# Kernel tuning notes

Measured on AMD Instinct MI355X. Metric: run time of the kernel, lower is better.

## Reference

```python
import jax, jax.numpy as jnp
import numpy as np

N, CDIM, FDIM, HDIM, K = 16384, 512, 512, 1024, 5
WEIGHT = 5.0
EPS = 1e-20


def _xavier(key, shape, gain):
    fan_in, fan_out = shape[-2], shape[-1]
    std = gain * np.sqrt(2.0 / (fan_in + fan_out))
    return jax.random.normal(key, shape, jnp.float32) * std


def setup_inputs() -> dict:
    key = jax.random.key(0)
    ks = jax.random.split(key, 12)
    g = np.sqrt(2.0)  # relu gain; last layer linear gain=1
    inp = {
        "c": jax.random.normal(ks[0], (N, CDIM), jnp.float32),
        "x": jax.random.normal(ks[1], (N, 3), jnp.float32),
        "noise": jax.random.normal(ks[2], (K, N, FDIM), jnp.float32),
        "gumbel_u": jax.random.uniform(ks[3], (N, K), jnp.float32),
        # probs MLP: cdim -> 1024 -> 1024 -> K
        "pw0": _xavier(ks[4], (CDIM, HDIM), g), "pb0": jnp.zeros((HDIM,), jnp.float32),
        "pw1": _xavier(ks[5], (HDIM, HDIM), g), "pb1": jnp.zeros((HDIM,), jnp.float32),
        "pw2": _xavier(ks[6], (HDIM, K), 1.0), "pb2": jnp.zeros((K,), jnp.float32),
        # K Gaussian MLPs (stacked): cdim -> 1024 -> 1024 -> 2*fdim
        "gw0": _xavier(ks[7], (K, CDIM, HDIM), g), "gb0": jnp.zeros((K, HDIM), jnp.float32),
        "gw1": _xavier(ks[8], (K, HDIM, HDIM), g), "gb1": jnp.zeros((K, HDIM), jnp.float32),
        "gw2": _xavier(ks[9], (K, HDIM, 2 * FDIM), 1.0), "gb2": jnp.zeros((K, 2 * FDIM), jnp.float32),
    }
    return inp


def reference(c, x, noise, gumbel_u, pw0, pb0, pw1, pb1, pw2, pb2,
              gw0, gb0, gw1, gb1, gw2, gb2):
    # mixture probabilities: ps = softmax(probs(c))
    h = jax.nn.relu(c @ pw0 + pb0)
    h = jax.nn.relu(h @ pw1 + pb1)
    logits = h @ pw2 + pb2                      # (N, K)
    ps = jax.nn.softmax(logits, axis=-1)

    # all K Gaussian experts, vectorized over component axis k
    g = jax.nn.relu(jnp.einsum('nc,kch->knh', c, gw0) + gb0[:, None, :])
    g = jax.nn.relu(jnp.einsum('knh,khj->knj', g, gw1) + gb1[:, None, :])
    o = jnp.einsum('knh,khf->knf', g, gw2) + gb2[:, None, :]   # (K, N, 2*FDIM)
    mean, logvar = o[..., :FDIM], o[..., FDIM:]
    sample = mean + noise * jnp.exp(logvar * 0.5)              # (K, N, FDIM)

    # per-row categorical draw with p = ps (Gumbel-max, on-device)
    gumbel = -jnp.log(-jnp.log(gumbel_u + EPS) + EPS)
    idx = jnp.argmax(jnp.log(jax.lax.stop_gradient(ps) + EPS) + gumbel, axis=-1)

    mask = jax.nn.one_hot(idx, K, dtype=ps.dtype) * WEIGHT
    weights = (ps + mask) / (1.0 + WEIGHT)                     # (N, K)
    out = jnp.einsum('nk,knf->nf', weights, sample)            # (N, FDIM)
    return out
```

## Files before the change

### kernel.cpp

```cpp
#include <hip/hip_runtime.h>
#include <cstdint>
#include <cstddef>

#define N_ROWS 16384
#define CDIM_C 512
#define HDIM_C 1024
#define FDIM_C 512
#define KMIX 5

typedef unsigned short u16;
typedef __attribute__((ext_vector_type(8))) short bf16x8;
typedef __attribute__((ext_vector_type(4))) float f32x4;

__device__ __forceinline__ u16 f2bf(float x) {
  unsigned u = __float_as_uint(x);
  unsigned r = (u + 0x7fffu + ((u >> 16) & 1u)) >> 16;
  return (u16)r;
}
__device__ __forceinline__ float bf2f(u16 h) {
  return __uint_as_float(((unsigned)h) << 16);
}

__device__ __forceinline__ void gload_lds16(const void* g, void* l) {
  __builtin_amdgcn_global_load_lds((const __attribute__((address_space(1))) void*)g,
                                   (__attribute__((address_space(3))) void*)l,
                                   16, 0, 0);
}

__global__ void split3_kernel(const float* __restrict__ x, u16* __restrict__ P0,
                              u16* __restrict__ P1, u16* __restrict__ P2, size_t n) {
  for (size_t i = (size_t)blockIdx.x * 256 + threadIdx.x; i < n; i += (size_t)gridDim.x * 256) {
    const float v = x[i];
    const u16 h = f2bf(v); const float hf = bf2f(h);
    const u16 m = f2bf(v - hf); const float mf = bf2f(m);
    P0[i] = h; P1[i] = m; P2[i] = f2bf(v - hf - mf);
  }
}

template <int NP>
__global__ void transp_split_kernel(const float* __restrict__ W, u16* __restrict__ P0,
                                    u16* __restrict__ P1, u16* __restrict__ P2,
                                    int R, int C) {
  __shared__ float t[32][33];
  const int bz = blockIdx.z;
  const float* Wz = W + (size_t)bz * R * C;
  const size_t oofs = (size_t)bz * R * C;
  const int r0 = blockIdx.x * 32, c0 = blockIdx.y * 32;
  const int tx = threadIdx.x, ty = threadIdx.y;
#pragma unroll
  for (int i = 0; i < 4; ++i)
    t[ty + i * 8][tx] = Wz[(size_t)(r0 + ty + i * 8) * C + c0 + tx];
  __syncthreads();
#pragma unroll
  for (int i = 0; i < 4; ++i) {
    const int c = c0 + ty + i * 8, r = r0 + tx;
    const float x = t[tx][ty + i * 8];
    const size_t idx = oofs + (size_t)c * R + r;
    const u16 h = f2bf(x);
    P0[idx] = h;
    const float hf = bf2f(h);
    const u16 m = f2bf(x - hf);
    P1[idx] = m;
    if (NP >= 3) {
      const float mf = bf2f(m);
      P2[idx] = f2bf(x - hf - mf);
    }
  }
}

template <int NA, int NB, int NT, bool RELU, int OSPL>
__global__ __launch_bounds__(256, 2) void gemm_split(
    const u16* __restrict__ A0, const u16* __restrict__ A1, const u16* __restrict__ A2,
    const u16* __restrict__ B0, const u16* __restrict__ B1, const u16* __restrict__ B2,
    const float* __restrict__ bias, float* __restrict__ outF,
    u16* __restrict__ O0, u16* __restrict__ O1, u16* __restrict__ O2,
    int M, int Nc, int Kd) {
  __shared__ u16 lds[(NA + NB) * 4096];
  const int tid = threadIdx.x;
  const int lane = tid & 63;
  const int wave = tid >> 6;
  const int wm = wave >> 1, wn = wave & 1;
  const int col0 = blockIdx.x * 128;
  const int row0 = blockIdx.y * 128;
  const u16* Ap[3] = {A0, A1, A2};
  const u16* Bp[3] = {B0, B1, B2};
  constexpr int TA[6] = {0, 0, 1, 1, 0, 2};
  constexpr int TB[6] = {0, 1, 0, 1, 2, 0};

  f32x4 acc[4][4] = {};
  const int kb = lane >> 4;
  const int rl = lane & 15;
  const int nSteps = Kd >> 5;

  for (int kt = 0; kt < nSteps; ++kt) {
    const int k0 = kt << 5;
    __syncthreads();
#pragma unroll
    for (int p = 0; p < NA + NB; ++p) {
      const u16* gp = (p < NA) ? Ap[p] : Bp[p - NA];
      const int rb = (p < NA) ? row0 : col0;
      u16* lbase = &lds[p * 4096];
#pragma unroll
      for (int it = 0; it < 2; ++it) {
        const int sbase = it * 256 + wave * 64;
        const int slot = sbase + lane;
        const int skb = slot >> 7;
        const int sr = slot & 127;
        const u16* src = gp + (size_t)(rb + sr) * Kd + (k0 + skb * 8);
        gload_lds16(src, lbase + sbase * 8);
      }
    }
    __syncthreads();

    bf16x8 aF[NA][4];
    bf16x8 bF[NB][4];
#pragma unroll
    for (int p = 0; p < NA; ++p)
#pragma unroll
      for (int i = 0; i < 4; ++i) {
        const int r = wm * 64 + i * 16 + rl;
        aF[p][i] = *(const bf16x8*)&lds[p * 4096 + (kb * 128 + r) * 8];
      }
#pragma unroll
    for (int p = 0; p < NB; ++p)
#pragma unroll
      for (int j = 0; j < 4; ++j) {
        const int r = wn * 64 + j * 16 + rl;
        bF[p][j] = *(const bf16x8*)&lds[(NA + p) * 4096 + (kb * 128 + r) * 8];
      }
#pragma unroll
    for (int t = 0; t < NT; ++t)
#pragma unroll
      for (int i = 0; i < 4; ++i)
#pragma unroll
        for (int j = 0; j < 4; ++j)
          acc[i][j] = __builtin_amdgcn_mfma_f32_16x16x32_bf16(
              aF[TA[t]][i], bF[TB[t]][j], acc[i][j], 0, 0, 0);
  }

#pragma unroll
  for (int i = 0; i < 4; ++i)
#pragma unroll
    for (int j = 0; j < 4; ++j)
#pragma unroll
      for (int r = 0; r < 4; ++r) {
        const int row = row0 + wm * 64 + i * 16 + (lane >> 4) * 4 + r;
        const int col = col0 + wn * 64 + j * 16 + (lane & 15);
        float y = acc[i][j][r] + bias[col];
        if (RELU) y = fmaxf(y, 0.0f);
        const size_t idx = (size_t)row * Nc + col;
        if constexpr (OSPL == 0) {
          outF[idx] = y;
        } else {
          const u16 h = f2bf(y);
          const float hf = bf2f(h);
          const u16 m = f2bf(y - hf);
          O0[idx] = h;
          O1[idx] = m;
          if constexpr (OSPL == 3) {
            const float mf = bf2f(m);
            O2[idx] = f2bf(y - hf - mf);
          }
        }
      }
  (void)M;
}

__global__ void p2_weights_kernel(const float* __restrict__ h2, const float* __restrict__ pw2,
                                  const float* __restrict__ pb2, const float* __restrict__ gu,
                                  float* __restrict__ w) {
  const int n = blockIdx.x * 4 + (threadIdx.x >> 6);
  const int lane = threadIdx.x & 63;
  const float* hrow = h2 + (size_t)n * HDIM_C;
  double acc[KMIX] = {0, 0, 0, 0, 0};
  const int c0 = lane * 16;
#pragma unroll
  for (int jj = 0; jj < 16; ++jj) {
    const int cc = c0 + jj;
    const double hv = (double)hrow[cc];
#pragma unroll
    for (int kk = 0; kk < KMIX; ++kk)
      acc[kk] += hv * (double)pw2[cc * KMIX + kk];
  }
#pragma unroll
  for (int offs = 32; offs >= 1; offs >>= 1)
#pragma unroll
    for (int kk = 0; kk < KMIX; ++kk)
      acc[kk] += __shfl_down(acc[kk], offs);
  if (lane == 0) {
    double lg[KMIX], mx = -1e300;
#pragma unroll
    for (int kk = 0; kk < KMIX; ++kk) {
      lg[kk] = acc[kk] + (double)pb2[kk];
      if (lg[kk] > mx) mx = lg[kk];
    }
    double e[KMIX], s = 0.0;
#pragma unroll
    for (int kk = 0; kk < KMIX; ++kk) { e[kk] = exp(lg[kk] - mx); s += e[kk]; }
    int idx = 0; double zb = -1e300;
#pragma unroll
    for (int kk = 0; kk < KMIX; ++kk) {
      const double ps = e[kk] / s;
      const double u = (double)gu[n * KMIX + kk];
      const double g = -log(-log(u + 1e-20) + 1e-20);
      const double zz = log(ps + 1e-20) + g;
      if (zz > zb) { zb = zz; idx = kk; }
    }
#pragma unroll
    for (int kk = 0; kk < KMIX; ++kk)
      w[n * KMIX + kk] = (float)((e[kk] / s + (kk == idx ? 5.0 : 0.0)) / 6.0);
  }
}

template <bool FIRST>
__global__ void mix_kernel(const float* __restrict__ o, const float* __restrict__ nz,
                           const float* __restrict__ w, float* __restrict__ out, int k) {
  const int i = blockIdx.x * 256 + threadIdx.x;
  const int n = i >> 7;
  const int fv = i & 127;
  const float wk = w[n * KMIX + k];
  const float4 me = *(const float4*)(o + (size_t)n * HDIM_C + fv * 4);
  const float4 lv = *(const float4*)(o + (size_t)n * HDIM_C + FDIM_C + fv * 4);
  const float4 nv = *(const float4*)(nz + (size_t)n * FDIM_C + fv * 4);
  float4 r;
  r.x = wk * (me.x + nv.x * expf(0.5f * lv.x));
  r.y = wk * (me.y + nv.y * expf(0.5f * lv.y));
  r.z = wk * (me.z + nv.z * expf(0.5f * lv.z));
  r.w = wk * (me.w + nv.w * expf(0.5f * lv.w));
  float4* op = (float4*)out + i;
  if (FIRST) {
    *op = r;
  } else {
    float4 p = *op;
    p.x += r.x; p.y += r.y; p.z += r.z; p.w += r.w;
    *op = p;
  }
}

extern "C" void kernel_launch(void* const* d_in, const int* in_sizes, int n_in,
                              void* d_out, int out_size, void* d_ws, size_t ws_size,
                              hipStream_t stream) {
  const float* c   = (const float*)d_in[0];
  const float* noise = (const float*)d_in[2];
  const float* gu  = (const float*)d_in[3];
  const float* pw0 = (const float*)d_in[4];
  const float* pb0 = (const float*)d_in[5];
  const float* pw1 = (const float*)d_in[6];
  const float* pb1 = (const float*)d_in[7];
  const float* pw2 = (const float*)d_in[8];
  const float* pb2 = (const float*)d_in[9];
  const float* gw0 = (const float*)d_in[10];
  const float* gb0 = (const float*)d_in[11];
  const float* gw1 = (const float*)d_in[12];
  const float* gb1 = (const float*)d_in[13];
  const float* gw2 = (const float*)d_in[14];
  const float* gb2 = (const float*)d_in[15];
  float* out = (float*)d_out;

  char* ws = (char*)d_ws;
  size_t off = 0;
  auto alloc = [&](size_t bytes) -> char* {
    off = (off + 255) & ~(size_t)255;
    char* p = ws + off;
    off += bytes;
    return p;
  };

  const size_t NCp = (size_t)N_ROWS * CDIM_C * 2;
  const size_t NHp = (size_t)N_ROWS * HDIM_C * 2;
  u16* cH = (u16*)alloc(NCp);
  u16* cM = (u16*)alloc(NCp);
  u16* cL = (u16*)alloc(NCp);
  u16* pw0T0 = (u16*)alloc((size_t)CDIM_C * HDIM_C * 2);
  u16* pw0T1 = (u16*)alloc((size_t)CDIM_C * HDIM_C * 2);
  u16* pw0T2 = (u16*)alloc((size_t)CDIM_C * HDIM_C * 2);
  u16* pw1T0 = (u16*)alloc((size_t)HDIM_C * HDIM_C * 2);
  u16* pw1T1 = (u16*)alloc((size_t)HDIM_C * HDIM_C * 2);
  u16* pw1T2 = (u16*)alloc((size_t)HDIM_C * HDIM_C * 2);
  u16* hH = (u16*)alloc(NHp);
  u16* hM = (u16*)alloc(NHp);
  u16* hL = (u16*)alloc(NHp);
  float* h2 = (float*)alloc((size_t)N_ROWS * HDIM_C * 4);
  float* wbuf = (float*)alloc((size_t)N_ROWS * KMIX * 4);
  u16* gw0T0 = (u16*)alloc((size_t)KMIX * CDIM_C * HDIM_C * 2);
  u16* gw0T1 = (u16*)alloc((size_t)KMIX * CDIM_C * HDIM_C * 2);
  u16* gw1T0 = (u16*)alloc((size_t)KMIX * HDIM_C * HDIM_C * 2);
  u16* gw1T1 = (u16*)alloc((size_t)KMIX * HDIM_C * HDIM_C * 2);
  u16* gw2T0 = (u16*)alloc((size_t)KMIX * HDIM_C * HDIM_C * 2);
  u16* gw2T1 = (u16*)alloc((size_t)KMIX * HDIM_C * HDIM_C * 2);
  u16* g2b = (u16*)alloc(NHp);
  u16* g1a = hH;
  u16* g1b = hM;
  u16* g2a = hL;
  float* obuf = h2;
  (void)ws_size; (void)in_sizes; (void)n_in; (void)out_size;

  split3_kernel<<<2048, 256, 0, stream>>>(c, cH, cM, cL, (size_t)N_ROWS * CDIM_C);
  transp_split_kernel<3><<<dim3(CDIM_C / 32, HDIM_C / 32, 1), dim3(32, 8), 0, stream>>>(
      pw0, pw0T0, pw0T1, pw0T2, CDIM_C, HDIM_C);
  transp_split_kernel<3><<<dim3(HDIM_C / 32, HDIM_C / 32, 1), dim3(32, 8), 0, stream>>>(
      pw1, pw1T0, pw1T1, pw1T2, HDIM_C, HDIM_C);
  transp_split_kernel<2><<<dim3(CDIM_C / 32, HDIM_C / 32, KMIX), dim3(32, 8), 0, stream>>>(
      gw0, gw0T0, gw0T1, nullptr, CDIM_C, HDIM_C);
  transp_split_kernel<2><<<dim3(HDIM_C / 32, HDIM_C / 32, KMIX), dim3(32, 8), 0, stream>>>(
      gw1, gw1T0, gw1T1, nullptr, HDIM_C, HDIM_C);
  transp_split_kernel<2><<<dim3(HDIM_C / 32, HDIM_C / 32, KMIX), dim3(32, 8), 0, stream>>>(
      gw2, gw2T0, gw2T1, nullptr, HDIM_C, HDIM_C);

  const dim3 gg(HDIM_C / 128, N_ROWS / 128);

  gemm_split<3, 3, 6, true, 3><<<gg, 256, 0, stream>>>(
      cH, cM, cL, pw0T0, pw0T1, pw0T2, pb0, nullptr, hH, hM, hL,
      N_ROWS, HDIM_C, CDIM_C);
  gemm_split<3, 3, 6, true, 0><<<gg, 256, 0, stream>>>(
      hH, hM, hL, pw1T0, pw1T1, pw1T2, pb1, h2, nullptr, nullptr, nullptr,
      N_ROWS, HDIM_C, HDIM_C);
  p2_weights_kernel<<<N_ROWS / 4, 256, 0, stream>>>(h2, pw2, pb2, gu, wbuf);

  for (int k = 0; k < KMIX; ++k) {
    gemm_split<2, 2, 3, true, 2><<<gg, 256, 0, stream>>>(
        cH, cM, nullptr,
        gw0T0 + (size_t)k * CDIM_C * HDIM_C, gw0T1 + (size_t)k * CDIM_C * HDIM_C, nullptr,
        gb0 + k * HDIM_C, nullptr, g1a, g1b, nullptr,
        N_ROWS, HDIM_C, CDIM_C);
    gemm_split<2, 2, 3, true, 2><<<gg, 256, 0, stream>>>(
        g1a, g1b, nullptr,
        gw1T0 + (size_t)k * HDIM_C * HDIM_C, gw1T1 + (size_t)k * HDIM_C * HDIM_C, nullptr,
        gb1 + k * HDIM_C, nullptr, g2a, g2b, nullptr,
        N_ROWS, HDIM_C, HDIM_C);
    gemm_split<2, 2, 3, false, 0><<<gg, 256, 0, stream>>>(
        g2a, g2b, nullptr,
        gw2T0 + (size_t)k * HDIM_C * HDIM_C, gw2T1 + (size_t)k * HDIM_C * HDIM_C, nullptr,
        gb2 + k * HDIM_C, obuf, nullptr, nullptr, nullptr,
        N_ROWS, HDIM_C, HDIM_C);
    if (k == 0)
      mix_kernel<true><<<N_ROWS * 128 / 256, 256, 0, stream>>>(
          obuf, noise + (size_t)k * N_ROWS * FDIM_C, wbuf, out, k);
    else
      mix_kernel<false><<<N_ROWS * 128 / 256, 256, 0, stream>>>(
          obuf, noise + (size_t)k * N_ROWS * FDIM_C, wbuf, out, k);
  }
}
```

Measured before the change: 2.639 ms.

## Fuse mixture sampling into last expert GEMM epilogue and swizzle workgroups

The columns of the last-layer expert weights are interleaved during transposition, so each mean/logvar pair lands in adjacent lanes. The GEMM epilogue then computes the reparameterised sample with a lane shuffle and accumulates the weighted result into the output directly. This removes the separate mix kernel and the full fp32 round trip of the expert output. It also adds an XCD-style workgroup remap for L2 locality and raises launch-bounds occupancy hints (3 or 4 blocks per CU), which risks register spills. Half the epilogue lanes sit idle and the output stores become strided.

```diff
diff --git a/kernel.cpp b/kernel.cpp
--- a/kernel.cpp
+++ b/kernel.cpp
@@ -37,7 +37,7 @@
   }
 }
 
-template <int NP>
+template <int NP, bool PERM>
 __global__ void transp_split_kernel(const float* __restrict__ W, u16* __restrict__ P0,
                                     u16* __restrict__ P1, u16* __restrict__ P2,
                                     int R, int C) {
@@ -53,7 +53,8 @@
   __syncthreads();
 #pragma unroll
   for (int i = 0; i < 4; ++i) {
-    const int c = c0 + ty + i * 8, r = r0 + tx;
+    const int c_raw = c0 + ty + i * 8, r = r0 + tx;
+    const int c = PERM ? ((c_raw < FDIM_C) ? (c_raw * 2) : ((c_raw - FDIM_C) * 2 + 1)) : c_raw;
     const float x = t[tx][ty + i * 8];
     const size_t idx = oofs + (size_t)c * R + r;
     const u16 h = f2bf(x);
@@ -68,20 +69,28 @@
   }
 }
 
-template <int NA, int NB, int NT, bool RELU, int OSPL>
-__global__ __launch_bounds__(256, 2) void gemm_split(
+template <int NA, int NB, int NT, bool RELU, int OSPL, int MIX, int BPC>
+__global__ __launch_bounds__(256, BPC) void gemm_split(
     const u16* __restrict__ A0, const u16* __restrict__ A1, const u16* __restrict__ A2,
     const u16* __restrict__ B0, const u16* __restrict__ B1, const u16* __restrict__ B2,
     const float* __restrict__ bias, float* __restrict__ outF,
     u16* __restrict__ O0, u16* __restrict__ O1, u16* __restrict__ O2,
+    const float* __restrict__ noise_k, const float* __restrict__ wvec,
+    float* __restrict__ mixout, int kidx,
     int M, int Nc, int Kd) {
   __shared__ u16 lds[(NA + NB) * 4096];
   const int tid = threadIdx.x;
   const int lane = tid & 63;
   const int wave = tid >> 6;
   const int wm = wave >> 1, wn = wave & 1;
-  const int col0 = blockIdx.x * 128;
-  const int row0 = blockIdx.y * 128;
+
+  const int nwg = (int)(gridDim.x * gridDim.y);
+  const int orig = (int)(blockIdx.y * gridDim.x + blockIdx.x);
+  const int cpx = nwg >> 3;
+  const int wg = (orig & 7) * cpx + (orig >> 3);
+  const int col0 = (wg & 7) * 128;
+  const int row0 = (wg >> 3) * 128;
+
   const u16* Ap[3] = {A0, A1, A2};
   const u16* Bp[3] = {B0, B1, B2};
   constexpr int TA[6] = {0, 0, 1, 1, 0, 2};
@@ -146,20 +155,33 @@
       for (int r = 0; r < 4; ++r) {
         const int row = row0 + wm * 64 + i * 16 + (lane >> 4) * 4 + r;
         const int col = col0 + wn * 64 + j * 16 + (lane & 15);
-        float y = acc[i][j][r] + bias[col];
-        if (RELU) y = fmaxf(y, 0.0f);
-        const size_t idx = (size_t)row * Nc + col;
-        if constexpr (OSPL == 0) {
-          outF[idx] = y;
+        if constexpr (MIX > 0) {
+          const int f = col >> 1;
+          const int ocol = (col & 1) ? (f + FDIM_C) : f;
+          const float y = acc[i][j][r] + bias[ocol];
+          const float other = __shfl_xor(y, 1);
+          if (!(lane & 1)) {
+            const float sample = y + noise_k[(size_t)row * FDIM_C + f] * expf(0.5f * other);
+            const float v = wvec[row * KMIX + kidx] * sample;
+            float* op = &mixout[(size_t)row * FDIM_C + f];
+            if constexpr (MIX == 1) *op = v; else *op += v;
+          }
         } else {
-          const u16 h = f2bf(y);
-          const float hf = bf2f(h);
-          const u16 m = f2bf(y - hf);
-          O0[idx] = h;
-          O1[idx] = m;
-          if constexpr (OSPL == 3) {
-            const float mf = bf2f(m);
-            O2[idx] = f2bf(y - hf - mf);
+          float y = acc[i][j][r] + bias[col];
+          if (RELU) y = fmaxf(y, 0.0f);
+          const size_t idx = (size_t)row * Nc + col;
+          if constexpr (OSPL == 0) {
+            outF[idx] = y;
+          } else {
+            const u16 h = f2bf(y);
+            const float hf = bf2f(h);
+            const u16 m = f2bf(y - hf);
+            O0[idx] = h;
+            O1[idx] = m;
+            if constexpr (OSPL == 3) {
+              const float mf = bf2f(m);
+              O2[idx] = f2bf(y - hf - mf);
+            }
           }
         }
       }
@@ -209,31 +231,6 @@
 #pragma unroll
     for (int kk = 0; kk < KMIX; ++kk)
       w[n * KMIX + kk] = (float)((e[kk] / s + (kk == idx ? 5.0 : 0.0)) / 6.0);
-  }
-}
-
-template <bool FIRST>
-__global__ void mix_kernel(const float* __restrict__ o, const float* __restrict__ nz,
-                           const float* __restrict__ w, float* __restrict__ out, int k) {
-  const int i = blockIdx.x * 256 + threadIdx.x;
-  const int n = i >> 7;
-  const int fv = i & 127;
-  const float wk = w[n * KMIX + k];
-  const float4 me = *(const float4*)(o + (size_t)n * HDIM_C + fv * 4);
-  const float4 lv = *(const float4*)(o + (size_t)n * HDIM_C + FDIM_C + fv * 4);
-  const float4 nv = *(const float4*)(nz + (size_t)n * FDIM_C + fv * 4);
-  float4 r;
-  r.x = wk * (me.x + nv.x * expf(0.5f * lv.x));
-  r.y = wk * (me.y + nv.y * expf(0.5f * lv.y));
-  r.z = wk * (me.z + nv.z * expf(0.5f * lv.z));
-  r.w = wk * (me.w + nv.w * expf(0.5f * lv.w));
-  float4* op = (float4*)out + i;
-  if (FIRST) {
-    *op = r;
-  } else {
-    float4 p = *op;
-    p.x += r.x; p.y += r.y; p.z += r.z; p.w += r.w;
-    *op = p;
   }
 }
 
@@ -292,52 +289,52 @@
   u16* g1a = hH;
   u16* g1b = hM;
   u16* g2a = hL;
-  float* obuf = h2;
   (void)ws_size; (void)in_sizes; (void)n_in; (void)out_size;
 
   split3_kernel<<<2048, 256, 0, stream>>>(c, cH, cM, cL, (size_t)N_ROWS * CDIM_C);
-  transp_split_kernel<3><<<dim3(CDIM_C / 32, HDIM_C / 32, 1), dim3(32, 8), 0, stream>>>(
+  transp_split_kernel<3, false><<<dim3(CDIM_C / 32, HDIM_C / 32, 1), dim3(32, 8), 0, stream>>>(
       pw0, pw0T0, pw0T1, pw0T2, CDIM_C, HDIM_C);
-  transp_split_kernel<3><<<dim3(HDIM_C / 32, HDIM_C / 32, 1), dim3(32, 8), 0, stream>>>(
+  transp_split_kernel<3, false><<<dim3(HDIM_C / 32, HDIM_C / 32, 1), dim3(32, 8), 0, stream>>>(
       pw1, pw1T0, pw1T1, pw1T2, HDIM_C, HDIM_C);
-  transp_split_kernel<2><<<dim3(CDIM_C / 32, HDIM_C / 32, KMIX), dim3(32, 8), 0, stream>>>(
+  transp_split_kernel<2, false><<<dim3(CDIM_C / 32, HDIM_C / 32, KMIX), dim3(32, 8), 0, stream>>>(
       gw0, gw0T0, gw0T1, nullptr, CDIM_C, HDIM_C);
-  transp_split_kernel<2><<<dim3(HDIM_C / 32, HDIM_C / 32, KMIX), dim3(32, 8), 0, stream>>>(
+  transp_split_kernel<2, false><<<dim3(HDIM_C / 32, HDIM_C / 32, KMIX), dim3(32, 8), 0, stream>>>(
       gw1, gw1T0, gw1T1, nullptr, HDIM_C, HDIM_C);
-  transp_split_kernel<2><<<dim3(HDIM_C / 32, HDIM_C / 32, KMIX), dim3(32, 8), 0, stream>>>(
+  transp_split_kernel<2, true><<<dim3(HDIM_C / 32, HDIM_C / 32, KMIX), dim3(32, 8), 0, stream>>>(
       gw2, gw2T0, gw2T1, nullptr, HDIM_C, HDIM_C);
 
   const dim3 gg(HDIM_C / 128, N_ROWS / 128);
 
-  gemm_split<3, 3, 6, true, 3><<<gg, 256, 0, stream>>>(
+  gemm_split<3, 3, 6, true, 3, 0, 3><<<gg, 256, 0, stream>>>(
       cH, cM, cL, pw0T0, pw0T1, pw0T2, pb0, nullptr, hH, hM, hL,
-      N_ROWS, HDIM_C, CDIM_C);
-  gemm_split<3, 3, 6, true, 0><<<gg, 256, 0, stream>>>(
+      nullptr, nullptr, nullptr, 0, N_ROWS, HDIM_C, CDIM_C);
+  gemm_split<3, 3, 6, true, 0, 0, 3><<<gg, 256, 0, stream>>>(
       hH, hM, hL, pw1T0, pw1T1, pw1T2, pb1, h2, nullptr, nullptr, nullptr,
-      N_ROWS, HDIM_C, HDIM_C);
+      nullptr, nullptr, nullptr, 0, N_ROWS, HDIM_C, HDIM_C);
   p2_weights_kernel<<<N_ROWS / 4, 256, 0, stream>>>(h2, pw2, pb2, gu, wbuf);
 
   for (int k = 0; k < KMIX; ++k) {
-    gemm_split<2, 2, 3, true, 2><<<gg, 256, 0, stream>>>(
+    gemm_split<2, 2, 3, true, 2, 0, 4><<<gg, 256, 0, stream>>>(
         cH, cM, nullptr,
         gw0T0 + (size_t)k * CDIM_C * HDIM_C, gw0T1 + (size_t)k * CDIM_C * HDIM_C, nullptr,
         gb0 + k * HDIM_C, nullptr, g1a, g1b, nullptr,
-        N_ROWS, HDIM_C, CDIM_C);
-    gemm_split<2, 2, 3, true, 2><<<gg, 256, 0, stream>>>(
+        nullptr, nullptr, nullptr, 0, N_ROWS, HDIM_C, CDIM_C);
+    gemm_split<2, 2, 3, true, 2, 0, 4><<<gg, 256, 0, stream>>>(
         g1a, g1b, nullptr,
         gw1T0 + (size_t)k * HDIM_C * HDIM_C, gw1T1 + (size_t)k * HDIM_C * HDIM_C, nullptr,
         gb1 + k * HDIM_C, nullptr, g2a, g2b, nullptr,
-        N_ROWS, HDIM_C, HDIM_C);
-    gemm_split<2, 2, 3, false, 0><<<gg, 256, 0, stream>>>(
-        g2a, g2b, nullptr,
-        gw2T0 + (size_t)k * HDIM_C * HDIM_C, gw2T1 + (size_t)k * HDIM_C * HDIM_C, nullptr,
-        gb2 + k * HDIM_C, obuf, nullptr, nullptr, nullptr,
-        N_ROWS, HDIM_C, HDIM_C);
+        nullptr, nullptr, nullptr, 0, N_ROWS, HDIM_C, HDIM_C);
     if (k == 0)
-      mix_kernel<true><<<N_ROWS * 128 / 256, 256, 0, stream>>>(
-          obuf, noise + (size_t)k * N_ROWS * FDIM_C, wbuf, out, k);
+      gemm_split<2, 2, 3, false, 0, 1, 4><<<gg, 256, 0, stream>>>(
+          g2a, g2b, nullptr,
+          gw2T0 + (size_t)k * HDIM_C * HDIM_C, gw2T1 + (size_t)k * HDIM_C * HDIM_C, nullptr,
+          gb2 + k * HDIM_C, nullptr, nullptr, nullptr, nullptr,
+          noise + (size_t)k * N_ROWS * FDIM_C, wbuf, out, k, N_ROWS, HDIM_C, HDIM_C);
     else
-      mix_kernel<false><<<N_ROWS * 128 / 256, 256, 0, stream>>>(
-          obuf, noise + (size_t)k * N_ROWS * FDIM_C, wbuf, out, k);
-  }
-}
+      gemm_split<2, 2, 3, false, 0, 2, 4><<<gg, 256, 0, stream>>>(
+          g2a, g2b, nullptr,
+          gw2T0 + (size_t)k * HDIM_C * HDIM_C, gw2T1 + (size_t)k * HDIM_C * HDIM_C, nullptr,
+          gb2 + k * HDIM_C, nullptr, nullptr, nullptr, nullptr,
+          noise + (size_t)k * N_ROWS * FDIM_C, wbuf, out, k, N_ROWS, HDIM_C, HDIM_C);
+  }
+}
```

After: 2.470 ms. 1.07x faster.
